# Optimization experiments

Hardware: AMD Instinct MI355X
Metric: run time of the kernel (lower is better)

## Reference

```python
import jax, jax.numpy as jnp
import numpy as np

# Network dimensions (match init_kwargs)
N_IN, N_HID, N_OUT = 2048, 8192, 1024
N = N_IN + N_HID + N_OUT
BATCH = 512


def setup_inputs() -> dict:
    key = jax.random.key(0)
    k_w, k_b, k_x = jax.random.split(key, 3)
    # GraphNet._init_connections: Xavier-ish std based on (n_inputs + n_outputs)
    std = (2.0 / (N_IN + N_OUT)) ** 0.5
    W = jax.random.normal(k_w, (N, N), dtype=jnp.float32) * std
    # mask: inputs -> hidden, hidden -> outputs (fixed 3-level DAG)
    mask = jnp.zeros((N, N), dtype=jnp.float32)
    mask = mask.at[:N_IN, N_IN:N_IN + N_HID].set(1.0)
    mask = mask.at[N_IN:N_IN + N_HID, N_IN + N_HID:].set(1.0)
    # bias is zero-init in the module; use small random values so it is exercised
    bias = jax.random.normal(k_b, (N,), dtype=jnp.float32) * 0.01
    x = jax.random.normal(k_x, (BATCH, N_IN), dtype=jnp.float32)
    return {"x": x, "W": W, "bias": bias, "mask": mask}


def reference(x, W, bias, mask):
    # Faithful translation of GraphNet.forward for the canonical 3-level
    # topology produced by _init_connections/_compute_levels:
    #   level 0: input nodes [0, N_IN)
    #   level 1: hidden nodes [N_IN, N_IN+N_HID)  -> ReLU
    #   level 2: output nodes [N_IN+N_HID, N)     -> identity (OUTPUT type)
    W_eff = W * mask                       # [N, N] masked adjacency
    B = x.shape[0]
    h = jnp.zeros((B, N), dtype=x.dtype).at[:, :N_IN].set(x)
    # level 1 (hidden): pre_act = h @ W_eff[:, idx] + bias[idx]; ReLU
    pre_h = h @ W_eff[:, N_IN:N_IN + N_HID] + bias[N_IN:N_IN + N_HID]
    h = h.at[:, N_IN:N_IN + N_HID].set(jax.nn.relu(pre_h))
    # level 2 (outputs): pre-activation only (node_type == OUTPUT -> no ReLU)
    pre_o = h @ W_eff[:, N_IN + N_HID:] + bias[N_IN + N_HID:]
    return pre_o                            # h[:, output_indices]
```

## Files before the change

kernel.cpp:

```cpp
#include <hip/hip_runtime.h>

#define N_IN 2048
#define N_HID 8192
#define N_OUT 1024
#define NTOT 11264

typedef __attribute__((ext_vector_type(4))) float f32x4;
typedef __attribute__((ext_vector_type(4))) short short4v;
typedef __attribute__((ext_vector_type(8))) short short8v;
typedef __attribute__((ext_vector_type(2))) unsigned u32x2;

__device__ inline short f2bf(float f) {
    unsigned u = __float_as_uint(f);
    return (short)((u + 0x7fffu + ((u >> 16) & 1u)) >> 16);
}

__device__ inline float bf2f(short s) {
    return __uint_as_float(((unsigned)(unsigned short)s) << 16);
}

__device__ inline unsigned cvt_pk_bf16(float lo, float hi) {
    unsigned r;
    asm("v_cvt_pk_bf16_f32 %0, %1, %2" : "=v"(r) : "v"(lo), "v"(hi));
    return r;
}

__device__ inline int perm64(int c) {
    return (c & 32) + (((c >> 2) & 3) << 3) + (((c >> 4) & 1) << 2) + (c & 3);
}

__device__ inline void gload_lds16(const void* g, void* l) {
    __builtin_amdgcn_global_load_lds(
        (const __attribute__((address_space(1))) unsigned int*)g,
        (__attribute__((address_space(3))) unsigned int*)l, 16, 0, 0);
}

#define WAITV(N) { asm volatile("s_waitcnt vmcnt(" #N ")" ::: "memory"); \
                   __builtin_amdgcn_sched_barrier(0); }
#define BARRIER  { asm volatile("s_waitcnt lgkmcnt(0)" ::: "memory"); \
                   __builtin_amdgcn_sched_barrier(0); \
                   __builtin_amdgcn_s_barrier(); \
                   __builtin_amdgcn_sched_barrier(0); }

__global__ __launch_bounds__(256) void cvt_x(
    const float* __restrict__ x, short* __restrict__ xb)
{
    const int i = blockIdx.x * 256 + threadIdx.x;
    const f32x4 v = *reinterpret_cast<const f32x4*>(x + (size_t)i * 4);
    u32x2 s;
    s[0] = cvt_pk_bf16(v[0], v[1]);
    s[1] = cvt_pk_bf16(v[2], v[3]);
    const int c0  = (i * 4) & (N_IN - 1);
    const int p   = (c0 & ~63) + perm64(c0 & 63);
    const size_t row = (size_t)(i >> 9);
    *reinterpret_cast<u32x2*>(xb + row * N_IN + p) = s;
}

__global__ __launch_bounds__(512, 2) void gemm1(
    const short* __restrict__ A,
    const float* __restrict__ W,
    const float* __restrict__ bias,
    short* __restrict__ hOut)
{
    __shared__ __align__(16) short As[4][128 * 64];
    __shared__ __align__(16) short Bs[2][128][72];

    const int bid = blockIdx.x;
    const int xcd = bid & 7;
    const int j   = bid >> 3;
    const int bx  = xcd * 8 + (j >> 2);
    const int by  = j & 3;

    const int t    = threadIdx.x;
    const int lane = t & 63;
    const int wid  = t >> 6;
    const int wr   = wid >> 2;
    const int wc   = wid & 3;
    const int brow = by * 128;
    const int bcol = bx * 128;
    const int l15  = lane & 15;
    const int lg   = lane >> 4;

    const int arow = lane >> 3;
    const int asw  = ((lane & 7) * 16) ^ (arow << 4);

    const int nb   = (lane & 7) + 8 * (wid >> 1);
    const int kblk = ((lane >> 3) & 7) + 8 * (wid & 1);
    const int n0 = nb * 4, k0 = kblk * 4;
    const int p0 = perm64(k0);

    const char*  Abytes = (const char*)A;
    const size_t lda_b  = (size_t)N_IN * 2;

    f32x4 acc[4][2] = {};
    f32x4 bv0[4], bv1[4], bv2[4], bv3[4];

    const float* wp0 = &W[(size_t)k0 * NTOT + (N_IN + bcol + n0)];

#define B_LOAD(TT, BV) { \
    const float* wp = wp0 + (size_t)(TT) * 64 * NTOT; \
    _Pragma("unroll") for (int jj = 0; jj < 4; ++jj) \
        BV[jj] = *reinterpret_cast<const f32x4*>(wp + (size_t)jj * NTOT); }

#define A_LOAD(TT) { \
    char* dst = (char*)As + ((TT) & 3) * 16384; \
    _Pragma("unroll") for (int i = 0; i < 2; ++i) { \
        const int c = wid * 2 + i; \
        gload_lds16(Abytes + (size_t)(brow + c * 8 + arow) * lda_b \
                          + (size_t)((TT) * 64) * 2 + asw, \
                    dst + c * 1024); } }

#define B_WRITE(TT, BV) { \
    short* bsb = &Bs[(TT) & 1][0][0]; \
    _Pragma("unroll") for (int i = 0; i < 4; ++i) { \
        u32x2 s; \
        s[0] = cvt_pk_bf16(BV[0][i], BV[1][i]); \
        s[1] = cvt_pk_bf16(BV[2][i], BV[3][i]); \
        *reinterpret_cast<u32x2*>(bsb + (n0 + i) * 72 + p0) = s; } }

#define COMPUTE(TT) { \
    const char*  ab = (const char*)As + ((TT) & 3) * 16384; \
    const short* bb = &Bs[(TT) & 1][0][0]; \
    short8v a[2][4], b[2][2]; \
    _Pragma("unroll") for (int g = 0; g < 2; ++g) { \
        const int koff = g * 64 + lg * 16; \
        _Pragma("unroll") for (int m = 0; m < 4; ++m) { \
            const int r = wr * 64 + m * 16 + l15; \
            a[g][m] = *reinterpret_cast<const short8v*>( \
                ab + ((r * 128 + koff) ^ ((r & 7) << 4))); } \
        _Pragma("unroll") for (int n = 0; n < 2; ++n) { \
            const int r = wc * 32 + n * 16 + l15; \
            b[g][n] = *reinterpret_cast<const short8v*>( \
                (const char*)(bb + r * 72) + koff); } } \
    __builtin_amdgcn_s_setprio(1); \
    _Pragma("unroll") for (int g = 0; g < 2; ++g) \
      _Pragma("unroll") for (int m = 0; m < 4; ++m) \
        _Pragma("unroll") for (int n = 0; n < 2; ++n) \
            acc[m][n] = __builtin_amdgcn_mfma_f32_16x16x32_bf16( \
                a[g][m], b[g][n], acc[m][n], 0, 0, 0); \
    __builtin_amdgcn_s_setprio(0); }

#define ITER(T, BVL, BVW) { \
    B_LOAD(T + 3, BVL); A_LOAD(T + 3); \
    WAITV(12); \
    B_WRITE(T + 1, BVW); \
    COMPUTE(T); \
    BARRIER; }

    B_LOAD(0, bv0); A_LOAD(0);
    B_LOAD(1, bv1); A_LOAD(1);
    B_LOAD(2, bv2); A_LOAD(2);
    WAITV(12);
    B_WRITE(0, bv0);
    BARRIER;

    const int nt = 32;
    for (int tt = 0; tt + 4 < nt; tt += 4) {
        ITER(tt,     bv3, bv1);
        ITER(tt + 1, bv0, bv2);
        ITER(tt + 2, bv1, bv3);
        ITER(tt + 3, bv2, bv0);
    }
    ITER(nt - 4, bv3, bv1);

    WAITV(6);
    B_WRITE(nt - 2, bv2);
    COMPUTE(nt - 3);
    BARRIER;
    WAITV(0);
    B_WRITE(nt - 1, bv3);
    COMPUTE(nt - 2);
    BARRIER;
    COMPUTE(nt - 1);

#undef B_LOAD
#undef A_LOAD
#undef B_WRITE
#undef COMPUTE
#undef ITER

#pragma unroll
    for (int m = 0; m < 4; ++m) {
        const int row0 = brow + wr * 64 + m * 16 + lg * 4;
#pragma unroll
        for (int n = 0; n < 2; ++n) {
            const int col  = bcol + wc * 32 + n * 16 + l15;
            const int pcol = (col & ~63) + perm64(col & 63);
            const float bb = bias[N_IN + col];
#pragma unroll
            for (int q = 0; q < 4; ++q) {
                float v = acc[m][n][q] + bb;
                v = v > 0.f ? v : 0.f;
                hOut[(size_t)(row0 + q) * N_HID + pcol] = f2bf(v);
            }
        }
    }
}

__global__ __launch_bounds__(512, 2) void gemm2(
    const short* __restrict__ A,
    const float* __restrict__ W,
    short* __restrict__ pOut)
{
    __shared__ __align__(16) short As[4][256 * 64];
    __shared__ __align__(16) short Bs[2][64][72];

    const int bid = blockIdx.x;
    const int bz  = bid & 7;
    const int j   = bid >> 3;
    const int bx  = j >> 1;
    const int by  = j & 1;

    const int t    = threadIdx.x;
    const int lane = t & 63;
    const int wid  = t >> 6;
    const int wr   = wid >> 1;
    const int wc   = wid & 1;
    const int brow = by * 256;
    const int bcol = bx * 64;
    const int l15  = lane & 15;
    const int lg   = lane >> 4;
    const int ks   = bz * 1024;

    const int arow = lane >> 3;
    const int asw  = ((lane & 7) * 16) ^ (arow << 4);

    const int k2 = (t >> 4) * 2;
    const int n0 = (t & 15) * 4;
    const int p2 = perm64(k2);

    const char*  Abytes = (const char*)A;
    const size_t lda_b  = (size_t)N_HID * 2;

    f32x4 acc[4][2] = {};
    f32x4 bv0[2], bv1[2], bv2[2], bv3[2];

    const float* wp0 = &W[(size_t)(N_IN + ks + k2) * NTOT
                          + (N_IN + N_HID + bcol + n0)];

#define B_LOAD(TT, BV) { \
    const float* wp = wp0 + (size_t)(TT) * 64 * NTOT; \
    BV[0] = *reinterpret_cast<const f32x4*>(wp); \
    BV[1] = *reinterpret_cast<const f32x4*>(wp + NTOT); }

#define A_LOAD(TT) { \
    char* dst = (char*)As + ((TT) & 3) * 32768; \
    _Pragma("unroll") for (int i = 0; i < 4; ++i) { \
        const int c = wid * 4 + i; \
        gload_lds16(Abytes + (size_t)(brow + c * 8 + arow) * lda_b \
                          + (size_t)(ks + (TT) * 64) * 2 + asw, \
                    dst + c * 1024); } }

#define B_WRITE(TT, BV) { \
    short* bsb = &Bs[(TT) & 1][0][0]; \
    _Pragma("unroll") for (int i = 0; i < 4; ++i) { \
        unsigned s = cvt_pk_bf16(BV[0][i], BV[1][i]); \
        *reinterpret_cast<unsigned*>(bsb + (n0 + i) * 72 + p2) = s; } }

#define COMPUTE(TT) { \
    const char*  ab = (const char*)As + ((TT) & 3) * 32768; \
    const short* bb = &Bs[(TT) & 1][0][0]; \
    short8v a[2][4], b[2][2]; \
    _Pragma("unroll") for (int g = 0; g < 2; ++g) { \
        const int koff = g * 64 + lg * 16; \
        _Pragma("unroll") for (int m = 0; m < 4; ++m) { \
            const int r = wr * 64 + m * 16 + l15; \
            a[g][m] = *reinterpret_cast<const short8v*>( \
                ab + ((r * 128 + koff) ^ ((r & 7) << 4))); } \
        _Pragma("unroll") for (int n = 0; n < 2; ++n) { \
            const int r = wc * 32 + n * 16 + l15; \
            b[g][n] = *reinterpret_cast<const short8v*>( \
                (const char*)(bb + r * 72) + koff); } } \
    __builtin_amdgcn_s_setprio(1); \
    _Pragma("unroll") for (int g = 0; g < 2; ++g) \
      _Pragma("unroll") for (int m = 0; m < 4; ++m) \
        _Pragma("unroll") for (int n = 0; n < 2; ++n) \
            acc[m][n] = __builtin_amdgcn_mfma_f32_16x16x32_bf16( \
                a[g][m], b[g][n], acc[m][n], 0, 0, 0); \
    __builtin_amdgcn_s_setprio(0); }

#define ITER(T, BVL, BVW) { \
    B_LOAD(T + 3, BVL); A_LOAD(T + 3); \
    WAITV(12); \
    B_WRITE(T + 1, BVW); \
    COMPUTE(T); \
    BARRIER; }

    B_LOAD(0, bv0); A_LOAD(0);
    B_LOAD(1, bv1); A_LOAD(1);
    B_LOAD(2, bv2); A_LOAD(2);
    WAITV(12);
    B_WRITE(0, bv0);
    BARRIER;

    const int nt = 16;
    for (int tt = 0; tt + 4 < nt; tt += 4) {
        ITER(tt,     bv3, bv1);
        ITER(tt + 1, bv0, bv2);
        ITER(tt + 2, bv1, bv3);
        ITER(tt + 3, bv2, bv0);
    }
    ITER(nt - 4, bv3, bv1);

    WAITV(6);
    B_WRITE(nt - 2, bv2);
    COMPUTE(nt - 3);
    BARRIER;
    WAITV(0);
    B_WRITE(nt - 1, bv3);
    COMPUTE(nt - 2);
    BARRIER;
    COMPUTE(nt - 1);

#undef B_LOAD
#undef A_LOAD
#undef B_WRITE
#undef COMPUTE
#undef ITER

    short* po = pOut + (size_t)bz * (512 * N_OUT);
#pragma unroll
    for (int m = 0; m < 4; ++m) {
        const int row0 = brow + wr * 64 + m * 16 + lg * 4;
#pragma unroll
        for (int n = 0; n < 2; ++n) {
            const int col = bcol + wc * 32 + n * 16 + l15;
#pragma unroll
            for (int q = 0; q < 4; ++q)
                po[(size_t)(row0 + q) * N_OUT + col] = f2bf(acc[m][n][q]);
        }
    }
}

__global__ __launch_bounds__(256) void reduce_bias(
    const short* __restrict__ part,
    const float* __restrict__ bias,
    float* __restrict__ out)
{
    const int idx = (blockIdx.x * 256 + threadIdx.x) * 4;
    f32x4 s = *reinterpret_cast<const f32x4*>(&bias[N_IN + N_HID + (idx & 1023)]);
#pragma unroll
    for (int sp = 0; sp < 8; ++sp) {
        const short4v p = *reinterpret_cast<const short4v*>(
            &part[(size_t)sp * 524288 + idx]);
#pragma unroll
        for (int jj = 0; jj < 4; ++jj) s[jj] += bf2f(p[jj]);
    }
    *reinterpret_cast<f32x4*>(&out[idx]) = s;
}

extern "C" void kernel_launch(void* const* d_in, const int* in_sizes, int n_in,
                              void* d_out, int out_size, void* d_ws, size_t ws_size,
                              hipStream_t stream) {
    const float* x    = (const float*)d_in[0];
    const float* W    = (const float*)d_in[1];
    const float* bias = (const float*)d_in[2];
    float* out = (float*)d_out;

    short* h    = (short*)d_ws;
    short* part = (short*)((char*)d_ws + (size_t)(8 << 20));
    short* xb   = (short*)((char*)d_ws + (size_t)(8 << 20));

    cvt_x<<<dim3(1024), dim3(256), 0, stream>>>(x, xb);

    gemm1<<<dim3(256), dim3(512), 0, stream>>>(xb, W, bias, h);

    gemm2<<<dim3(256), dim3(512), 0, stream>>>(h, W, part);

    reduce_bias<<<dim3(512), dim3(256), 0, stream>>>(part, bias, out);
}
```

Measured before the change: 66.74 us.

## Fuse x fp32-to-bf16 conversion into gemm1 and retile gemm2 to 128x128

Drops the separate cvt_x kernel. gemm1 now loads fp32 x rows through registers, converts them to bf16 and writes them into swizzled LDS, with a new three-stage B and two-stage A register pipeline. gemm2 is retiled from 256x64 to 128x128 output tiles with an XCD-aware block mapping and a wider per-thread B load. This removes one launch and a workspace round trip, at the cost of more registers and VALU work in gemm1 and the loss of async direct-to-LDS loads for A there.

```diff
diff --git a/kernel.cpp b/kernel.cpp
--- a/kernel.cpp
+++ b/kernel.cpp
@@ -42,27 +42,13 @@
                    __builtin_amdgcn_s_barrier(); \
                    __builtin_amdgcn_sched_barrier(0); }
 
-__global__ __launch_bounds__(256) void cvt_x(
-    const float* __restrict__ x, short* __restrict__ xb)
-{
-    const int i = blockIdx.x * 256 + threadIdx.x;
-    const f32x4 v = *reinterpret_cast<const f32x4*>(x + (size_t)i * 4);
-    u32x2 s;
-    s[0] = cvt_pk_bf16(v[0], v[1]);
-    s[1] = cvt_pk_bf16(v[2], v[3]);
-    const int c0  = (i * 4) & (N_IN - 1);
-    const int p   = (c0 & ~63) + perm64(c0 & 63);
-    const size_t row = (size_t)(i >> 9);
-    *reinterpret_cast<u32x2*>(xb + row * N_IN + p) = s;
-}
-
 __global__ __launch_bounds__(512, 2) void gemm1(
-    const short* __restrict__ A,
+    const float* __restrict__ x,
     const float* __restrict__ W,
     const float* __restrict__ bias,
     short* __restrict__ hOut)
 {
-    __shared__ __align__(16) short As[4][128 * 64];
+    __shared__ __align__(16) short As[2][128 * 64];
     __shared__ __align__(16) short Bs[2][128][72];
 
     const int bid = blockIdx.x;
@@ -81,21 +67,186 @@
     const int l15  = lane & 15;
     const int lg   = lane >> 4;
 
-    const int arow = lane >> 3;
-    const int asw  = ((lane & 7) * 16) ^ (arow << 4);
+    const int ar = t >> 2;
+    const int kq = (t & 3) * 16;
+    const int pbase = ((kq & 32) + ((kq >> 4) & 1) * 4) * 2;
+    const int arx = (ar & 7) << 4;
+    const float* xrow = x + (size_t)(brow + ar) * N_IN + kq;
 
     const int nb   = (lane & 7) + 8 * (wid >> 1);
     const int kblk = ((lane >> 3) & 7) + 8 * (wid & 1);
     const int n0 = nb * 4, k0 = kblk * 4;
     const int p0 = perm64(k0);
 
+    f32x4 acc[4][2] = {};
+    f32x4 bv0[4], bv1[4], bv2[4];
+    f32x4 av0[4], av1[4];
+
+    const float* wp0 = &W[(size_t)k0 * NTOT + (N_IN + bcol + n0)];
+
+#define B_LOAD(TT, BV) { \
+    const float* wp = wp0 + (size_t)(TT) * 64 * NTOT; \
+    _Pragma("unroll") for (int jj = 0; jj < 4; ++jj) \
+        BV[jj] = *reinterpret_cast<const f32x4*>(wp + (size_t)jj * NTOT); }
+
+#define A_LOADR(TT, AV) { \
+    const float* xp = xrow + (TT) * 64; \
+    _Pragma("unroll") for (int jj = 0; jj < 4; ++jj) \
+        AV[jj] = *reinterpret_cast<const f32x4*>(xp + jj * 4); }
+
+#define A_WRITE(TT, AV) { \
+    char* dst = (char*)As + ((TT) & 1) * 16384; \
+    _Pragma("unroll") for (int jj = 0; jj < 4; ++jj) { \
+        u32x2 s; \
+        s[0] = cvt_pk_bf16(AV[jj][0], AV[jj][1]); \
+        s[1] = cvt_pk_bf16(AV[jj][2], AV[jj][3]); \
+        *reinterpret_cast<u32x2*>( \
+            dst + ((ar * 128 + pbase + jj * 16) ^ arx)) = s; } }
+
+#define B_WRITE(TT, BV) { \
+    short* bsb = &Bs[(TT) & 1][0][0]; \
+    _Pragma("unroll") for (int i = 0; i < 4; ++i) { \
+        u32x2 s; \
+        s[0] = cvt_pk_bf16(BV[0][i], BV[1][i]); \
+        s[1] = cvt_pk_bf16(BV[2][i], BV[3][i]); \
+        *reinterpret_cast<u32x2*>(bsb + (n0 + i) * 72 + p0) = s; } }
+
+#define COMPUTE(TT) { \
+    const char*  ab = (const char*)As + ((TT) & 1) * 16384; \
+    const short* bb = &Bs[(TT) & 1][0][0]; \
+    short8v a[2][4], b[2][2]; \
+    _Pragma("unroll") for (int g = 0; g < 2; ++g) { \
+        const int koff = g * 64 + lg * 16; \
+        _Pragma("unroll") for (int m = 0; m < 4; ++m) { \
+            const int r = wr * 64 + m * 16 + l15; \
+            a[g][m] = *reinterpret_cast<const short8v*>( \
+                ab + ((r * 128 + koff) ^ ((r & 7) << 4))); } \
+        _Pragma("unroll") for (int n = 0; n < 2; ++n) { \
+            const int r = wc * 32 + n * 16 + l15; \
+            b[g][n] = *reinterpret_cast<const short8v*>( \
+                (const char*)(bb + r * 72) + koff); } } \
+    __builtin_amdgcn_s_setprio(1); \
+    _Pragma("unroll") for (int g = 0; g < 2; ++g) \
+      _Pragma("unroll") for (int m = 0; m < 4; ++m) \
+        _Pragma("unroll") for (int n = 0; n < 2; ++n) \
+            acc[m][n] = __builtin_amdgcn_mfma_f32_16x16x32_bf16( \
+                a[g][m], b[g][n], acc[m][n], 0, 0, 0); \
+    __builtin_amdgcn_s_setprio(0); }
+
+#define ITER(T, BVL, AVL, AVW, BVW) { \
+    B_LOAD(T + 3, BVL); \
+    A_LOADR(T + 2, AVL); \
+    WAITV(8); \
+    A_WRITE(T + 1, AVW); \
+    B_WRITE(T + 1, BVW); \
+    COMPUTE(T); \
+    BARRIER; }
+
+    B_LOAD(0, bv0);
+    A_LOADR(0, av0);
+    B_LOAD(1, bv1);
+    A_LOADR(1, av1);
+    B_LOAD(2, bv2);
+    WAITV(12);
+    A_WRITE(0, av0);
+    B_WRITE(0, bv0);
+    BARRIER;
+
+    for (int tt = 0; tt < 24; tt += 6) {
+        ITER(tt,     bv0, av0, av1, bv1);
+        ITER(tt + 1, bv1, av1, av0, bv2);
+        ITER(tt + 2, bv2, av0, av1, bv0);
+        ITER(tt + 3, bv0, av1, av0, bv1);
+        ITER(tt + 4, bv1, av0, av1, bv2);
+        ITER(tt + 5, bv2, av1, av0, bv0);
+    }
+    ITER(24, bv0, av0, av1, bv1);
+    ITER(25, bv1, av1, av0, bv2);
+    ITER(26, bv2, av0, av1, bv0);
+    ITER(27, bv0, av1, av0, bv1);
+    ITER(28, bv1, av0, av1, bv2);
+
+    A_LOADR(31, av1);
+    WAITV(4);
+    A_WRITE(30, av0);
+    B_WRITE(30, bv0);
+    COMPUTE(29);
+    BARRIER;
+    WAITV(0);
+    A_WRITE(31, av1);
+    B_WRITE(31, bv1);
+    COMPUTE(30);
+    BARRIER;
+    COMPUTE(31);
+
+#undef B_LOAD
+#undef A_LOADR
+#undef A_WRITE
+#undef B_WRITE
+#undef COMPUTE
+#undef ITER
+
+#pragma unroll
+    for (int m = 0; m < 4; ++m) {
+        const int row0 = brow + wr * 64 + m * 16 + lg * 4;
+#pragma unroll
+        for (int n = 0; n < 2; ++n) {
+            const int col  = bcol + wc * 32 + n * 16 + l15;
+            const int pcol = (col & ~63) + perm64(col & 63);
+            const float bb = bias[N_IN + col];
+#pragma unroll
+            for (int q = 0; q < 4; ++q) {
+                float v = acc[m][n][q] + bb;
+                v = v > 0.f ? v : 0.f;
+                hOut[(size_t)(row0 + q) * N_HID + pcol] = f2bf(v);
+            }
+        }
+    }
+}
+
+__global__ __launch_bounds__(512, 2) void gemm2(
+    const short* __restrict__ A,
+    const float* __restrict__ W,
+    short* __restrict__ pOut)
+{
+    __shared__ __align__(16) short As[4][128 * 64];
+    __shared__ __align__(16) short Bs[2][128][72];
+
+    const int bid = blockIdx.x;
+    const int xcd = bid & 7;
+    const int j   = bid >> 3;
+    const int xz  = xcd * 8 + (j >> 2);
+    const int bx  = xz & 7;
+    const int bz  = xz >> 3;
+    const int by  = j & 3;
+
+    const int t    = threadIdx.x;
+    const int lane = t & 63;
+    const int wid  = t >> 6;
+    const int wr   = wid >> 2;
+    const int wc   = wid & 3;
+    const int brow = by * 128;
+    const int bcol = bx * 128;
+    const int l15  = lane & 15;
+    const int lg   = lane >> 4;
+    const int ks   = bz * 1024;
+
+    const int arow = lane >> 3;
+    const int asw  = ((lane & 7) * 16) ^ (arow << 4);
+
+    const int nb   = (lane & 7) + 8 * (wid >> 1);
+    const int kblk = ((lane >> 3) & 7) + 8 * (wid & 1);
+    const int n0 = nb * 4, k0 = kblk * 4;
+    const int p0 = perm64(k0);
+
     const char*  Abytes = (const char*)A;
-    const size_t lda_b  = (size_t)N_IN * 2;
+    const size_t lda_b  = (size_t)N_HID * 2;
 
     f32x4 acc[4][2] = {};
     f32x4 bv0[4], bv1[4], bv2[4], bv3[4];
 
-    const float* wp0 = &W[(size_t)k0 * NTOT + (N_IN + bcol + n0)];
+    const float* wp0 = &W[(size_t)(N_IN + ks + k0) * NTOT
+                          + (N_IN + N_HID + bcol + n0)];
 
 #define B_LOAD(TT, BV) { \
     const float* wp = wp0 + (size_t)(TT) * 64 * NTOT; \
@@ -107,7 +258,7 @@
     _Pragma("unroll") for (int i = 0; i < 2; ++i) { \
         const int c = wid * 2 + i; \
         gload_lds16(Abytes + (size_t)(brow + c * 8 + arow) * lda_b \
-                          + (size_t)((TT) * 64) * 2 + asw, \
+                          + (size_t)(ks + (TT) * 64) * 2 + asw, \
                     dst + c * 1024); } }
 
 #define B_WRITE(TT, BV) { \
@@ -154,145 +305,6 @@
     B_WRITE(0, bv0);
     BARRIER;
 
-    const int nt = 32;
-    for (int tt = 0; tt + 4 < nt; tt += 4) {
-        ITER(tt,     bv3, bv1);
-        ITER(tt + 1, bv0, bv2);
-        ITER(tt + 2, bv1, bv3);
-        ITER(tt + 3, bv2, bv0);
-    }
-    ITER(nt - 4, bv3, bv1);
-
-    WAITV(6);
-    B_WRITE(nt - 2, bv2);
-    COMPUTE(nt - 3);
-    BARRIER;
-    WAITV(0);
-    B_WRITE(nt - 1, bv3);
-    COMPUTE(nt - 2);
-    BARRIER;
-    COMPUTE(nt - 1);
-
-#undef B_LOAD
-#undef A_LOAD
-#undef B_WRITE
-#undef COMPUTE
-#undef ITER
-
-#pragma unroll
-    for (int m = 0; m < 4; ++m) {
-        const int row0 = brow + wr * 64 + m * 16 + lg * 4;
-#pragma unroll
-        for (int n = 0; n < 2; ++n) {
-            const int col  = bcol + wc * 32 + n * 16 + l15;
-            const int pcol = (col & ~63) + perm64(col & 63);
-            const float bb = bias[N_IN + col];
-#pragma unroll
-            for (int q = 0; q < 4; ++q) {
-                float v = acc[m][n][q] + bb;
-                v = v > 0.f ? v : 0.f;
-                hOut[(size_t)(row0 + q) * N_HID + pcol] = f2bf(v);
-            }
-        }
-    }
-}
-
-__global__ __launch_bounds__(512, 2) void gemm2(
-    const short* __restrict__ A,
-    const float* __restrict__ W,
-    short* __restrict__ pOut)
-{
-    __shared__ __align__(16) short As[4][256 * 64];
-    __shared__ __align__(16) short Bs[2][64][72];
-
-    const int bid = blockIdx.x;
-    const int bz  = bid & 7;
-    const int j   = bid >> 3;
-    const int bx  = j >> 1;
-    const int by  = j & 1;
-
-    const int t    = threadIdx.x;
-    const int lane = t & 63;
-    const int wid  = t >> 6;
-    const int wr   = wid >> 1;
-    const int wc   = wid & 1;
-    const int brow = by * 256;
-    const int bcol = bx * 64;
-    const int l15  = lane & 15;
-    const int lg   = lane >> 4;
-    const int ks   = bz * 1024;
-
-    const int arow = lane >> 3;
-    const int asw  = ((lane & 7) * 16) ^ (arow << 4);
-
-    const int k2 = (t >> 4) * 2;
-    const int n0 = (t & 15) * 4;
-    const int p2 = perm64(k2);
-
-    const char*  Abytes = (const char*)A;
-    const size_t lda_b  = (size_t)N_HID * 2;
-
-    f32x4 acc[4][2] = {};
-    f32x4 bv0[2], bv1[2], bv2[2], bv3[2];
-
-    const float* wp0 = &W[(size_t)(N_IN + ks + k2) * NTOT
-                          + (N_IN + N_HID + bcol + n0)];
-
-#define B_LOAD(TT, BV) { \
-    const float* wp = wp0 + (size_t)(TT) * 64 * NTOT; \
-    BV[0] = *reinterpret_cast<const f32x4*>(wp); \
-    BV[1] = *reinterpret_cast<const f32x4*>(wp + NTOT); }
-
-#define A_LOAD(TT) { \
-    char* dst = (char*)As + ((TT) & 3) * 32768; \
-    _Pragma("unroll") for (int i = 0; i < 4; ++i) { \
-        const int c = wid * 4 + i; \
-        gload_lds16(Abytes + (size_t)(brow + c * 8 + arow) * lda_b \
-                          + (size_t)(ks + (TT) * 64) * 2 + asw, \
-                    dst + c * 1024); } }
-
-#define B_WRITE(TT, BV) { \
-    short* bsb = &Bs[(TT) & 1][0][0]; \
-    _Pragma("unroll") for (int i = 0; i < 4; ++i) { \
-        unsigned s = cvt_pk_bf16(BV[0][i], BV[1][i]); \
-        *reinterpret_cast<unsigned*>(bsb + (n0 + i) * 72 + p2) = s; } }
-
-#define COMPUTE(TT) { \
-    const char*  ab = (const char*)As + ((TT) & 3) * 32768; \
-    const short* bb = &Bs[(TT) & 1][0][0]; \
-    short8v a[2][4], b[2][2]; \
-    _Pragma("unroll") for (int g = 0; g < 2; ++g) { \
-        const int koff = g * 64 + lg * 16; \
-        _Pragma("unroll") for (int m = 0; m < 4; ++m) { \
-            const int r = wr * 64 + m * 16 + l15; \
-            a[g][m] = *reinterpret_cast<const short8v*>( \
-                ab + ((r * 128 + koff) ^ ((r & 7) << 4))); } \
-        _Pragma("unroll") for (int n = 0; n < 2; ++n) { \
-            const int r = wc * 32 + n * 16 + l15; \
-            b[g][n] = *reinterpret_cast<const short8v*>( \
-                (const char*)(bb + r * 72) + koff); } } \
-    __builtin_amdgcn_s_setprio(1); \
-    _Pragma("unroll") for (int g = 0; g < 2; ++g) \
-      _Pragma("unroll") for (int m = 0; m < 4; ++m) \
-        _Pragma("unroll") for (int n = 0; n < 2; ++n) \
-            acc[m][n] = __builtin_amdgcn_mfma_f32_16x16x32_bf16( \
-                a[g][m], b[g][n], acc[m][n], 0, 0, 0); \
-    __builtin_amdgcn_s_setprio(0); }
-
-#define ITER(T, BVL, BVW) { \
-    B_LOAD(T + 3, BVL); A_LOAD(T + 3); \
-    WAITV(12); \
-    B_WRITE(T + 1, BVW); \
-    COMPUTE(T); \
-    BARRIER; }
-
-    B_LOAD(0, bv0); A_LOAD(0);
-    B_LOAD(1, bv1); A_LOAD(1);
-    B_LOAD(2, bv2); A_LOAD(2);
-    WAITV(12);
-    B_WRITE(0, bv0);
-    BARRIER;
-
     const int nt = 16;
     for (int tt = 0; tt + 4 < nt; tt += 4) {
         ITER(tt,     bv3, bv1);
@@ -359,11 +371,8 @@
 
     short* h    = (short*)d_ws;
     short* part = (short*)((char*)d_ws + (size_t)(8 << 20));
-    short* xb   = (short*)((char*)d_ws + (size_t)(8 << 20));
-
-    cvt_x<<<dim3(1024), dim3(256), 0, stream>>>(x, xb);
-
-    gemm1<<<dim3(256), dim3(512), 0, stream>>>(xb, W, bias, h);
+
+    gemm1<<<dim3(256), dim3(512), 0, stream>>>(x, W, bias, h);
 
     gemm2<<<dim3(256), dim3(512), 0, stream>>>(h, W, part);
 
```

After: 59.32 us (median of 2 runs). -11.1%, faster.
